# Performance work log

Hardware: AMD Instinct MI355X
Metric: run time of the kernel (lower is better)

## Reference

```python
import jax, jax.numpy as jnp
import numpy as np

KH, KW = 3, 3          # kernel_size
SH, SW = 1, 1          # stride
PH, PW = 1, 1          # padding
NCODEBOOKS = 16
SUBVEC = 36            # (64*3*3)/16
K = 16                 # codewords per codebook (4 tree levels)


def _unfold(x):
    """torch.nn.functional.unfold equivalent: (b,c,h,w) -> (b, c*KH*KW, oh, ow),
    feature dim ordered channel-major (c, ki, kj) like torch."""
    b, c, h, w = x.shape
    xp = jnp.pad(x, ((0, 0), (0, 0), (PH, PH), (PW, PW)))
    oh = (h + 2 * PH - KH) // SH + 1
    ow = (w + 2 * PW - KW) // SW + 1
    patches = [xp[:, :, i:i + (oh - 1) * SH + 1:SH, j:j + (ow - 1) * SW + 1:SW]
               for i in range(KH) for j in range(KW)]
    cols = jnp.stack(patches, axis=2)              # (b, c, KH*KW, oh, ow)
    return cols.reshape(b, c * KH * KW, oh, ow)


def setup_inputs() -> dict:
    key = jax.random.key(0)
    k1, k2, k3, k4, k5 = jax.random.split(key, 5)
    return {
        "x": jax.random.normal(k1, (16, 64, 56, 56), dtype=jnp.float32),
        "split_idxs": jax.random.randint(k2, (NCODEBOOKS, 4), 0, SUBVEC, dtype=jnp.int32),
        "split_vals": jax.random.normal(k3, (NCODEBOOKS, 4, K // 2), dtype=jnp.float32),
        "lookup_tables": jax.random.normal(k4, (NCODEBOOKS, K, 64), dtype=jnp.float32),
        "bias": jax.random.normal(k5, (64,), dtype=jnp.float32),
    }


def reference(x, split_idxs, split_vals, lookup_tables, bias):
    b = x.shape[0]
    cols = _unfold(x)                              # (b, d, oh, ow)
    _, d, oh, ow = cols.shape
    # torch: cols.permute(0,2,1).flatten(0,1) with L=oh*ow row-major
    xf = cols.reshape(b, d, oh * ow).transpose(0, 2, 1).reshape(-1, d)  # (n, d)
    n = xf.shape[0]
    xs = xf.reshape(n, NCODEBOOKS, SUBVEC)
    car = jnp.arange(NCODEBOOKS)
    # Hierarchical 4-level threshold encoding (vectorized over all codebooks):
    # at level t, a point in bucket e compares feature split_idxs[c,t] against
    # split_vals[c,t,e]; new bucket = 2*e + (v >= thr)  (matches the serial
    # bucket-list construction: '<' -> left child, '>=' -> right child).
    enc = jnp.zeros((n, NCODEBOOKS), dtype=jnp.int32)
    for t in range(4):
        v = xs[:, car, split_idxs[:, t]]           # (n, NCODEBOOKS)
        thr = split_vals[car[None, :], t, enc]     # (n, NCODEBOOKS)
        enc = 2 * enc + (v >= thr).astype(jnp.int32)
    # LUT gather-sum (equivalent to one_hot(enc) @ lookup_tables[i], summed)
    gathered = lookup_tables[car[None, :], enc]    # (n, NCODEBOOKS, out_ch)
    out = gathered.sum(axis=1) + bias              # (n, out_ch)
    out = out.reshape(b, oh, ow, -1).transpose(0, 3, 1, 2)
    return out
```

## Files before the change

kernel.cpp:

```cpp
#include <hip/hip_runtime.h>
#include <hip/hip_fp16.h>

static constexpr int W56 = 56;
static constexpr int SP  = 56 * 56;
static constexpr int CHN = 64;

__device__ __forceinline__ float rfl_f(float v) {
    return __int_as_float(__builtin_amdgcn_readfirstlane(__float_as_int(v)));
}

__global__ __launch_bounds__(256, 3) void maddness_fused(
    const float* __restrict__ x,
    const int*   __restrict__ si,
    const float* __restrict__ sv,
    const float* __restrict__ lut,
    const float* __restrict__ bias,
    float*       __restrict__ out)
{
    __shared__ __half2        lutLds[256 * 36];
    __shared__ unsigned short codes[256];

    const int tid  = threadIdx.x;
    const int part = tid >> 6;
    const int lane = tid & 63;

    const int p  = blockIdx.x * 64 + lane;
    const int b  = p / SP;
    const int s  = p - b * SP;
    const int y  = s / W56;
    const int xc = s - y * W56;
    const float* __restrict__ xb = x + b * (CHN * SP);

    float v[4][4];
    #pragma unroll
    for (int c = 0; c < 4; ++c) {
        #pragma unroll
        for (int t = 0; t < 4; ++t) {
            const int cb = part * 4 + c;
            const int i  = cb * 4 + t;
            const int g  = __builtin_amdgcn_readfirstlane(si[i]) + cb * 36;
            const int ch = g / 9;
            const int k9 = g - ch * 9;
            const int ki = k9 / 3;
            const int dy = ki - 1;
            const int dx = (k9 - ki * 3) - 1;
            const int yy = y + dy, xx = xc + dx;
            const bool ok = ((unsigned)yy < (unsigned)W56) & ((unsigned)xx < (unsigned)W56);
            const int yyc = min(max(yy, 0), W56 - 1);
            const int xxc = min(max(xx, 0), W56 - 1);
            const float lv = xb[ch * SP + yyc * W56 + xxc];
            v[c][t] = ok ? lv : 0.0f;
        }
    }

    const float4* lut4 = reinterpret_cast<const float4*>(lut);
    #pragma unroll
    for (int i = 0; i < 8; ++i) {
        const int idx = tid + i * 256;
        const int row = idx >> 3;
        const int ck  = idx & 7;
        const float4 f0 = lut4[idx * 2];
        const float4 f1 = lut4[idx * 2 + 1];
        __half2 h[4];
        h[0] = __float22half2_rn(make_float2(f0.x, f0.y));
        h[1] = __float22half2_rn(make_float2(f0.z, f0.w));
        h[2] = __float22half2_rn(make_float2(f1.x, f1.y));
        h[3] = __float22half2_rn(make_float2(f1.z, f1.w));
        *reinterpret_cast<float4*>(&lutLds[row * 36 + ck * 4]) = *reinterpret_cast<const float4*>(h);
    }

    float T0[4], T1[4][2], T2[4][4], T3[4][8];
    #pragma unroll
    for (int c = 0; c < 4; ++c) {
        const int base = (part * 4 + c) * 32;
        T0[c] = rfl_f(sv[base]);
        #pragma unroll
        for (int j = 0; j < 2; ++j) T1[c][j] = rfl_f(sv[base + 8  + j]);
        #pragma unroll
        for (int j = 0; j < 4; ++j) T2[c][j] = rfl_f(sv[base + 16 + j]);
        #pragma unroll
        for (int j = 0; j < 8; ++j) T3[c][j] = rfl_f(sv[base + 24 + j]);
    }

    unsigned code = 0;
    #pragma unroll
    for (int c = 0; c < 4; ++c) {
        const bool b0 = v[c][0] >= T0[c];
        const float t1 = b0 ? T1[c][1] : T1[c][0];
        const bool b1 = v[c][1] >= t1;
        const float s01 = b1 ? T2[c][1] : T2[c][0];
        const float s23 = b1 ? T2[c][3] : T2[c][2];
        const bool b2 = v[c][2] >= (b0 ? s23 : s01);
        const float w0 = b2 ? T3[c][1] : T3[c][0];
        const float w1 = b2 ? T3[c][3] : T3[c][2];
        const float w2 = b2 ? T3[c][5] : T3[c][4];
        const float w3 = b2 ? T3[c][7] : T3[c][6];
        const float z0 = b1 ? w1 : w0;
        const float z1 = b1 ? w3 : w2;
        const bool b3 = v[c][3] >= (b0 ? z1 : z0);
        const int e = ((int)b0 << 3) | ((int)b1 << 2) | ((int)b2 << 1) | (int)b3;
        code |= (unsigned)e << (4 * c);
    }
    codes[part * 64 + lane] = (unsigned short)code;
    __syncthreads();

    const int q = part;
    const unsigned cd0 = codes[lane];
    const unsigned cd1 = codes[64 + lane];
    const unsigned cd2 = codes[128 + lane];
    const unsigned cd3 = codes[192 + lane];

    __half2 acc[8];
    #pragma unroll
    for (int r = 0; r < 8; ++r) acc[r] = __half2{__half(0.0f), __half(0.0f)};

    #pragma unroll
    for (int cb = 0; cb < 16; ++cb) {
        const unsigned cw = (cb < 4) ? cd0 : (cb < 8) ? cd1 : (cb < 12) ? cd2 : cd3;
        const int e = (int)((cw >> ((cb & 3) * 4)) & 15u);
        const __half2* __restrict__ row = &lutLds[(cb * 16 + e) * 36 + q * 8];
        #pragma unroll
        for (int r = 0; r < 8; ++r) acc[r] += row[r];
    }

    float* __restrict__ op = out + b * (CHN * SP) + (q * 16) * SP + s;
    const float* __restrict__ bq = bias + q * 16;
    #pragma unroll
    for (int r = 0; r < 8; ++r) {
        const float2 f = __half22float2(acc[r]);
        op[(2 * r)     * SP] = f.x + bq[2 * r];
        op[(2 * r + 1) * SP] = f.y + bq[2 * r + 1];
    }
}

extern "C" void kernel_launch(void* const* d_in, const int* in_sizes, int n_in,
                              void* d_out, int out_size, void* d_ws, size_t ws_size,
                              hipStream_t stream) {
    const float* x  = (const float*)d_in[0];
    const int*   si = (const int*)  d_in[1];
    const float* sv = (const float*)d_in[2];
    const float* lt = (const float*)d_in[3];
    const float* bs = (const float*)d_in[4];
    float* o = (float*)d_out;

    maddness_fused<<<dim3(784), dim3(256), 0, stream>>>(x, si, sv, lt, bs, o);
}
```

Measured before the change: 76.26 us.

## Precompute fp16 swizzled LUT in prep kernel and async-copy it into LDS

Adds a small prep kernel that converts the lookup tables to fp16 once, in an XOR-swizzled 32-half2 row layout, and writes the result to workspace. The main kernel then fills LDS with global_load_lds direct copies instead of converting per block, and reads each LUT row with two 16-byte swizzled loads to avoid bank conflicts. It also trims the LDS footprint, raises the occupancy hint to 4 blocks per CU, and uses wave-uniform pointers instead of readfirstlane. The cost is an extra kernel launch and reliance on async LDS copy semantics without an explicit wait before the barrier.

```diff
diff --git a/kernel.cpp b/kernel.cpp
--- a/kernel.cpp
+++ b/kernel.cpp
@@ -5,24 +5,44 @@
 static constexpr int SP  = 56 * 56;
 static constexpr int CHN = 64;
 
-__device__ __forceinline__ float rfl_f(float v) {
-    return __int_as_float(__builtin_amdgcn_readfirstlane(__float_as_int(v)));
+__global__ __launch_bounds__(256) void lut_prep(const float* __restrict__ lut,
+                                                __half* __restrict__ wlut) {
+    const int t = blockIdx.x * 256 + threadIdx.x;
+    const int r = t >> 3;
+    const int c = (t & 7) ^ (r & 7);
+    const float4* src = reinterpret_cast<const float4*>(lut + r * 64 + c * 8);
+    const float4 f0 = src[0];
+    const float4 f1 = src[1];
+    __half2 h[4];
+    h[0] = __float22half2_rn(make_float2(f0.x, f0.y));
+    h[1] = __float22half2_rn(make_float2(f0.z, f0.w));
+    h[2] = __float22half2_rn(make_float2(f1.x, f1.y));
+    h[3] = __float22half2_rn(make_float2(f1.z, f1.w));
+    *reinterpret_cast<float4*>(wlut + t * 8) = *reinterpret_cast<const float4*>(h);
 }
 
-__global__ __launch_bounds__(256, 3) void maddness_fused(
-    const float* __restrict__ x,
-    const int*   __restrict__ si,
-    const float* __restrict__ sv,
-    const float* __restrict__ lut,
-    const float* __restrict__ bias,
-    float*       __restrict__ out)
+__device__ __forceinline__ void async_copy16(const void* g, void* l) {
+    __builtin_amdgcn_global_load_lds(
+        (const __attribute__((address_space(1))) void*)g,
+        (__attribute__((address_space(3))) void*)l,
+        16, 0, 0);
+}
+
+__global__ __launch_bounds__(256, 4) void maddness_fused(
+    const float*  __restrict__ x,
+    const int*    __restrict__ si,
+    const float*  __restrict__ sv,
+    const __half* __restrict__ wlut,
+    const float*  __restrict__ bias,
+    float*        __restrict__ out)
 {
-    __shared__ __half2        lutLds[256 * 36];
+    __shared__ __half2        lutLds[256 * 32];
     __shared__ unsigned short codes[256];
 
     const int tid  = threadIdx.x;
     const int part = tid >> 6;
     const int lane = tid & 63;
+    const int pu   = __builtin_amdgcn_readfirstlane(part);
 
     const int p  = blockIdx.x * 64 + lane;
     const int b  = p / SP;
@@ -31,14 +51,14 @@
     const int xc = s - y * W56;
     const float* __restrict__ xb = x + b * (CHN * SP);
 
+    const int* __restrict__ sip = si + pu * 16;
     float v[4][4];
     #pragma unroll
     for (int c = 0; c < 4; ++c) {
         #pragma unroll
         for (int t = 0; t < 4; ++t) {
-            const int cb = part * 4 + c;
-            const int i  = cb * 4 + t;
-            const int g  = __builtin_amdgcn_readfirstlane(si[i]) + cb * 36;
+            const int cb = pu * 4 + c;
+            const int g  = sip[c * 4 + t] + cb * 36;
             const int ch = g / 9;
             const int k9 = g - ch * 9;
             const int ki = k9 / 3;
@@ -53,33 +73,26 @@
         }
     }
 
-    const float4* lut4 = reinterpret_cast<const float4*>(lut);
-    #pragma unroll
-    for (int i = 0; i < 8; ++i) {
-        const int idx = tid + i * 256;
-        const int row = idx >> 3;
-        const int ck  = idx & 7;
-        const float4 f0 = lut4[idx * 2];
-        const float4 f1 = lut4[idx * 2 + 1];
-        __half2 h[4];
-        h[0] = __float22half2_rn(make_float2(f0.x, f0.y));
-        h[1] = __float22half2_rn(make_float2(f0.z, f0.w));
-        h[2] = __float22half2_rn(make_float2(f1.x, f1.y));
-        h[3] = __float22half2_rn(make_float2(f1.z, f1.w));
-        *reinterpret_cast<float4*>(&lutLds[row * 36 + ck * 4]) = *reinterpret_cast<const float4*>(h);
+    {
+        const char* gsrc = reinterpret_cast<const char*>(wlut) + pu * 8192 + lane * 16;
+        char*       ldst = reinterpret_cast<char*>(lutLds) + pu * 8192;
+        #pragma unroll
+        for (int i = 0; i < 8; ++i)
+            async_copy16(gsrc + i * 1024, ldst + i * 1024);
     }
 
+    const float* __restrict__ svp = sv + pu * 128;
     float T0[4], T1[4][2], T2[4][4], T3[4][8];
     #pragma unroll
     for (int c = 0; c < 4; ++c) {
-        const int base = (part * 4 + c) * 32;
-        T0[c] = rfl_f(sv[base]);
+        const int base = c * 32;
+        T0[c] = svp[base];
         #pragma unroll
-        for (int j = 0; j < 2; ++j) T1[c][j] = rfl_f(sv[base + 8  + j]);
+        for (int j = 0; j < 2; ++j) T1[c][j] = svp[base + 8  + j];
         #pragma unroll
-        for (int j = 0; j < 4; ++j) T2[c][j] = rfl_f(sv[base + 16 + j]);
+        for (int j = 0; j < 4; ++j) T2[c][j] = svp[base + 16 + j];
         #pragma unroll
-        for (int j = 0; j < 8; ++j) T3[c][j] = rfl_f(sv[base + 24 + j]);
+        for (int j = 0; j < 8; ++j) T3[c][j] = svp[base + 24 + j];
     }
 
     unsigned code = 0;
@@ -117,10 +130,21 @@
     #pragma unroll
     for (int cb = 0; cb < 16; ++cb) {
         const unsigned cw = (cb < 4) ? cd0 : (cb < 8) ? cd1 : (cb < 12) ? cd2 : cd3;
-        const int e = (int)((cw >> ((cb & 3) * 4)) & 15u);
-        const __half2* __restrict__ row = &lutLds[(cb * 16 + e) * 36 + q * 8];
+        const int e   = (int)((cw >> ((cb & 3) * 4)) & 15u);
+        const int row = cb * 16 + e;
+        const int swz = e & 7;
+        const int c0  = (2 * q) ^ swz;
+        const int c1  = c0 ^ 1;
+        const __half2* __restrict__ base = &lutLds[row * 32];
+        const float4 ra = *reinterpret_cast<const float4*>(base + c0 * 4);
+        const float4 rb = *reinterpret_cast<const float4*>(base + c1 * 4);
+        const __half2* ha = reinterpret_cast<const __half2*>(&ra);
+        const __half2* hb = reinterpret_cast<const __half2*>(&rb);
         #pragma unroll
-        for (int r = 0; r < 8; ++r) acc[r] += row[r];
+        for (int r = 0; r < 4; ++r) {
+            acc[r]     += ha[r];
+            acc[4 + r] += hb[r];
+        }
     }
 
     float* __restrict__ op = out + b * (CHN * SP) + (q * 16) * SP + s;
@@ -142,6 +166,8 @@
     const float* lt = (const float*)d_in[3];
     const float* bs = (const float*)d_in[4];
     float* o = (float*)d_out;
+    __half* wlut = (__half*)d_ws;
 
-    maddness_fused<<<dim3(784), dim3(256), 0, stream>>>(x, si, sv, lt, bs, o);
+    lut_prep<<<dim3(8), dim3(256), 0, stream>>>(lt, wlut);
+    maddness_fused<<<dim3(784), dim3(256), 0, stream>>>(x, si, sv, wlut, bs, o);
 }
```

New measurement: 77.07 us. Within noise of the previous version (+1.1%).
